# Optimization experiments

Hardware: AMD Instinct MI355X
Metric: run time of the kernel (lower is better)

The kernel has to match this reference:

```python
import jax, jax.numpy as jnp
import numpy as np

EPS_LN = 1e-5

def _ln(x, g, b):
    m = x.mean(-1, keepdims=True)
    v = jnp.var(x, axis=-1, keepdims=True)
    return (x - m) * jax.lax.rsqrt(v + EPS_LN) * g + b


def _forward(x, edge_attr, lin0_w, lin0_b, enn_w1, enn_b1, enn_g1, enn_b1n,
             enn_w2, enn_b2, enn_g2, enn_b2n, conv_bias,
             gru_w_ih, gru_w_hh, gru_b_ih, gru_b_hh,
             lstm_w_ih, lstm_w_hh, lstm_b_ih, lstm_b_hh,
             lin1_w, lin1_b, lin1_g, lin1_bn, lin2_w, lin2_b,
             edge_index, target_index, target_class):
    N = x.shape[0]
    D = lin0_w.shape[0]
    src, dst = edge_index[0], edge_index[1]

    out = jax.nn.relu(x @ lin0_w.T + lin0_b)            # [N, D]
    h = out                                             # GRU hidden state

    # edge NN -> per-edge weight matrix [E, D, D] (edge_attr constant across iters)
    e1 = jax.nn.relu(_ln(edge_attr @ enn_w1.T + enn_b1, enn_g1, enn_b1n))
    ew = _ln(e1 @ enn_w2.T + enn_b2, enn_g2, enn_b2n).reshape(-1, D, D)

    counts = jnp.clip(jax.ops.segment_sum(jnp.ones_like(dst, jnp.float32), dst, num_segments=N), 1.0)[:, None]

    for _ in range(3):
        msg = jnp.einsum('ed,edo->eo', out[src], ew)     # per-edge matmul
        agg = jax.ops.segment_sum(msg, dst, num_segments=N) / counts  # scatter-mean
        m = jax.nn.relu(agg + conv_bias)
        # GRU cell (seq len 1)
        gx = m @ gru_w_ih.T + gru_b_ih
        gh = h @ gru_w_hh.T + gru_b_hh
        xr, xz, xn = jnp.split(gx, 3, axis=-1)
        hr, hz, hn = jnp.split(gh, 3, axis=-1)
        r = jax.nn.sigmoid(xr + hr)
        z = jax.nn.sigmoid(xz + hz)
        n = jnp.tanh(xn + r * hn)
        h = (1.0 - z) * n + z * h
        out = h

    # Set2Set with batch_index = arange(N) (each node is its own set), 3 steps
    idx = jnp.arange(N)
    hl = jnp.zeros((N, D), x.dtype)
    cl = jnp.zeros((N, D), x.dtype)
    q_star = jnp.zeros((N, 2 * D), x.dtype)
    for _ in range(3):
        g = q_star @ lstm_w_ih.T + lstm_b_ih + hl @ lstm_w_hh.T + lstm_b_hh
        gi, gf, gg, go = jnp.split(g, 4, axis=-1)
        cl = jax.nn.sigmoid(gf) * cl + jax.nn.sigmoid(gi) * jnp.tanh(gg)
        hl = jax.nn.sigmoid(go) * jnp.tanh(cl)
        q = hl
        e = (out * q[idx]).sum(-1, keepdims=True)
        emax = jax.ops.segment_max(e, idx, num_segments=N)
        a = jnp.exp(e - emax[idx])
        a = a / (jax.ops.segment_sum(a, idx, num_segments=N)[idx] + 1e-16)
        r_pool = jax.ops.segment_sum(a * out, idx, num_segments=N)
        q_star = jnp.concatenate([q, r_pool], axis=-1)

    a0, a1 = target_index[0], target_index[1]
    cat = jnp.concatenate([out[a0], out[a1], q_star[a0], q_star[a1]], axis=-1)  # [P, 6D]
    p = jax.nn.relu(_ln(cat @ lin1_w.T + lin1_b, lin1_g, lin1_bn))
    p = p @ lin2_w.T + lin2_b                           # [P, 8]
    return jnp.take_along_axis(p, target_class[:, None], axis=1)[:, 0]


def setup_inputs() -> dict:
    N, E, P, F, D = 10000, 20000, 15000, 16, 64
    ks = iter(jax.random.split(jax.random.key(0), 40))
    def nrm(shape, s=0.1):
        return jax.random.normal(next(ks), shape, jnp.float32) * s
    return {
        'x': jax.random.normal(next(ks), (N, F), jnp.float32),
        'edge_attr': jax.random.normal(next(ks), (E, 4), jnp.float32),
        'lin0_w': nrm((D, F)), 'lin0_b': jnp.zeros((D,), jnp.float32),
        'enn_w1': nrm((128, 4)), 'enn_b1': jnp.zeros((128,), jnp.float32),
        'enn_g1': jnp.ones((128,), jnp.float32), 'enn_b1n': jnp.zeros((128,), jnp.float32),
        'enn_w2': nrm((D * D, 128), 0.05), 'enn_b2': jnp.zeros((D * D,), jnp.float32),
        'enn_g2': jnp.ones((D * D,), jnp.float32), 'enn_b2n': jnp.zeros((D * D,), jnp.float32),
        'conv_bias': jnp.zeros((D,), jnp.float32),
        'gru_w_ih': nrm((3 * D, D)), 'gru_w_hh': nrm((3 * D, D)),
        'gru_b_ih': jnp.zeros((3 * D,), jnp.float32), 'gru_b_hh': jnp.zeros((3 * D,), jnp.float32),
        'lstm_w_ih': nrm((4 * D, 2 * D)), 'lstm_w_hh': nrm((4 * D, D)),
        'lstm_b_ih': jnp.zeros((4 * D,), jnp.float32), 'lstm_b_hh': jnp.zeros((4 * D,), jnp.float32),
        'lin1_w': nrm((D, 6 * D)), 'lin1_b': jnp.zeros((D,), jnp.float32),
        'lin1_g': jnp.ones((D,), jnp.float32), 'lin1_bn': jnp.zeros((D,), jnp.float32),
        'lin2_w': nrm((8, D)), 'lin2_b': jnp.zeros((8,), jnp.float32),
        'edge_index': jax.random.randint(next(ks), (2, E), 0, N),
        'target_index': jax.random.randint(next(ks), (2, P), 0, N),
        'target_class': jax.random.randint(next(ks), (P,), 0, 8),
    }


def reference(x, edge_attr, lin0_w, lin0_b, enn_w1, enn_b1, enn_g1, enn_b1n,
              enn_w2, enn_b2, enn_g2, enn_b2n, conv_bias,
              gru_w_ih, gru_w_hh, gru_b_ih, gru_b_hh,
              lstm_w_ih, lstm_w_hh, lstm_b_ih, lstm_b_hh,
              lin1_w, lin1_b, lin1_g, lin1_bn, lin2_w, lin2_b,
              edge_index, target_index, target_class):
    return _forward(x, edge_attr, lin0_w, lin0_b, enn_w1, enn_b1, enn_g1, enn_b1n,
                    enn_w2, enn_b2, enn_g2, enn_b2n, conv_bias,
                    gru_w_ih, gru_w_hh, gru_b_ih, gru_b_hh,
                    lstm_w_ih, lstm_w_hh, lstm_b_ih, lstm_b_hh,
                    lin1_w, lin1_b, lin1_g, lin1_bn, lin2_w, lin2_b,
                    edge_index, target_index, target_class)
```

## Files before the change

kernel.cpp:

```cpp
#include <hip/hip_runtime.h>
#include <hip/hip_bf16.h>

#define EPS_LN 1e-5f

typedef __attribute__((ext_vector_type(8))) short bf16x8;
typedef __attribute__((ext_vector_type(4))) float f32x4;

__device__ __forceinline__ float dot4(float4 a, float4 b) {
    return a.x * b.x + a.y * b.y + a.z * b.z + a.w * b.w;
}
__device__ __forceinline__ float sigmoidf_(float x) { return 1.0f / (1.0f + expf(-x)); }

__device__ __forceinline__ float bfu2f(unsigned short u) {
    unsigned v = ((unsigned)u) << 16;
    float f;
    __builtin_memcpy(&f, &v, 4);
    return f;
}
__device__ __forceinline__ unsigned short f2bfu(float f) {
    __hip_bfloat16 h = __float2bfloat16(f);
    unsigned short u;
    __builtin_memcpy(&u, &h, 2);
    return u;
}
__device__ __forceinline__ unsigned pack2bf(float a, float b) {
    return (unsigned)f2bfu(a) | ((unsigned)f2bfu(b) << 16);
}

__global__ void init_kernel(const float* __restrict__ x, const float* __restrict__ w,
                            const float* __restrict__ b, float* __restrict__ h,
                            const int* __restrict__ ei, float* __restrict__ counts,
                            int N, int E) {
    int id = blockIdx.x * blockDim.x + threadIdx.x;
    if (id < N * 64) {
        int n = id >> 6, o = id & 63;
        const float* xr = x + n * 16;
        const float* wr = w + o * 16;
        float acc = b[o];
#pragma unroll
        for (int k = 0; k < 16; k++) acc += xr[k] * wr[k];
        h[id] = fmaxf(acc, 0.0f);
    }
    if (id < E) atomicAdd(&counts[ei[E + id]], 1.0f);
}

__global__ __launch_bounds__(128) void edge_nn1_kernel(
    const float* __restrict__ ea, const float* __restrict__ w1, const float* __restrict__ b1,
    const float* __restrict__ g1, const float* __restrict__ b1n,
    unsigned short* __restrict__ e1h, unsigned short* __restrict__ e1l, int E) {
    int e = blockIdx.x, j = threadIdx.x;
    float a0 = ea[e * 4 + 0], a1 = ea[e * 4 + 1], a2 = ea[e * 4 + 2], a3 = ea[e * 4 + 3];
    const float* wr = w1 + j * 4;
    float z = b1[j] + a0 * wr[0] + a1 * wr[1] + a2 * wr[2] + a3 * wr[3];
    float s = z, s2 = z * z;
#pragma unroll
    for (int m = 32; m >= 1; m >>= 1) { s += __shfl_xor(s, m); s2 += __shfl_xor(s2, m); }
    __shared__ float ls[2], ls2[2];
    int wv = j >> 6;
    if ((j & 63) == 0) { ls[wv] = s; ls2[wv] = s2; }
    __syncthreads();
    float S = ls[0] + ls[1], S2 = ls2[0] + ls2[1];
    float mu = S * (1.0f / 128.0f);
    float var = fmaxf(S2 * (1.0f / 128.0f) - mu * mu, 0.0f);
    float inv = rsqrtf(var + EPS_LN);
    float v = fmaxf((z - mu) * inv * g1[j] + b1n[j], 0.0f);
    unsigned short hi = f2bfu(v);
    unsigned short lo = f2bfu(v - bfu2f(hi));
    e1h[e * 128 + j] = hi;
    e1l[e * 128 + j] = lo;
}

__global__ __launch_bounds__(128) void mpart_kernel(const float* __restrict__ w2,
                                                    const float* __restrict__ b2,
                                                    const float* __restrict__ g2,
                                                    unsigned short* __restrict__ w2g,
                                                    float* __restrict__ b2g,
                                                    float* __restrict__ pMT, float* __restrict__ pv,
                                                    float* __restrict__ pcw, float* __restrict__ psb,
                                                    float* __restrict__ pc) {
    __shared__ float wL[16][128];
    __shared__ float b2L[16];
    int t = threadIdx.x, b = blockIdx.x;
#pragma unroll
    for (int i = 0; i < 16; i++) {
        int idx = t + i * 128;
        wL[idx >> 7][idx & 127] = w2[(size_t)(b * 16 + (idx >> 7)) * 128 + (idx & 127)];
    }
    if (t < 16) b2L[t] = b2[b * 16 + t];
    __syncthreads();
#pragma unroll
    for (int o = 0; o < 16; o++) {
        int row = b * 16 + o;
        w2g[(size_t)row * 128 + t] = f2bfu(wL[o][t] * g2[row]);
    }
    if (t < 16) b2g[b * 16 + t] = b2L[t] * g2[b * 16 + t];
    int j = t;
    float wj[16];
#pragma unroll
    for (int o = 0; o < 16; o++) wj[o] = wL[o][j];
    float pvj = 0.f, pcwj = 0.f;
#pragma unroll
    for (int o = 0; o < 16; o++) { pvj += wj[o] * b2L[o]; pcwj += wj[o]; }
    for (int i4 = 0; i4 < 32; i4++) {
        float4 a = {0.f, 0.f, 0.f, 0.f};
#pragma unroll
        for (int o = 0; o < 16; o++) {
            float4 w4 = *(const float4*)&wL[o][i4 * 4];
            a.x += wj[o] * w4.x; a.y += wj[o] * w4.y;
            a.z += wj[o] * w4.z; a.w += wj[o] * w4.w;
        }
        *(float4*)&pMT[((size_t)b * 128 + j) * 128 + i4 * 4] = a;
    }
    pv[b * 128 + j] = pvj;
    pcw[b * 128 + j] = pcwj;
    if (t == 0) {
        float sb = 0.f, cc = 0.f;
#pragma unroll
        for (int o = 0; o < 16; o++) { sb += b2L[o]; cc += b2L[o] * b2L[o]; }
        psb[b] = sb;
        pc[b] = cc;
    }
}

__global__ __launch_bounds__(256) void mreduce_kernel(const float* __restrict__ pMT,
                                                      const float* __restrict__ pv,
                                                      const float* __restrict__ pcw,
                                                      const float* __restrict__ psb,
                                                      const float* __restrict__ pc,
                                                      unsigned short* __restrict__ mb,
                                                      float* __restrict__ varr,
                                                      float* __restrict__ cw,
                                                      float* __restrict__ sbc) {
    int fid = blockIdx.x * 256 + threadIdx.x;
    float s = 0.f;
    int j = fid >> 7, i = fid & 127;
    for (int b = 0; b < 256; b++) s += pMT[((size_t)b * 128 + j) * 128 + i];
    mb[fid] = f2bfu(s);
    if (fid < 128) {
        float sv = 0.f, sc = 0.f;
        for (int b = 0; b < 256; b++) { sv += pv[b * 128 + fid]; sc += pcw[b * 128 + fid]; }
        varr[fid] = sv;
        cw[fid] = sc;
    }
    if (fid == 0) {
        float sb = 0.f, cc = 0.f;
        for (int b = 0; b < 256; b++) { sb += psb[b]; cc += pc[b]; }
        sbc[0] = sb;
        sbc[1] = cc;
    }
}

__global__ __launch_bounds__(256) void stats_kernel(
    const unsigned short* __restrict__ e1h, const unsigned short* __restrict__ e1l,
    const unsigned short* __restrict__ mb, const float* __restrict__ cw,
    const float* __restrict__ varr, const float* __restrict__ sbc,
    float* __restrict__ stats, int E) {
    __shared__ __align__(16) unsigned char smem[65536];
    const int t = threadIdx.x;
    const int eb = blockIdx.x * 64;
#pragma unroll
    for (int r = 0; r < 4; r++) {
        int idx = t + r * 256;
        int row = idx >> 4, kseg = idx & 15;
        int er = eb + row;
        if (er >= E) er = E - 1;
        uint4 vh = *(const uint4*)&e1h[(size_t)er * 128 + kseg * 8];
        uint4 vl = *(const uint4*)&e1l[(size_t)er * 128 + kseg * 8];
        int off = row * 256 + ((kseg * 16) ^ ((row & 7) << 4));
        *(uint4*)(smem + off) = vh;
        *(uint4*)(smem + 16384 + off) = vl;
    }
#pragma unroll
    for (int r = 0; r < 8; r++) {
        int idx = t + r * 256;
        int row = idx >> 4, kseg = idx & 15;
        uint4 v = *(const uint4*)&mb[(size_t)row * 128 + kseg * 8];
        *(uint4*)(smem + 32768 + row * 256 + ((kseg * 16) ^ ((row & 7) << 4))) = v;
    }
    __syncthreads();
    const int w = t >> 6, lane = t & 63;
    const int wrow = w * 16;
    const int r16 = lane & 15, kg = lane >> 4;
    f32x4 tacc[8];
#pragma unroll
    for (int nj = 0; nj < 8; nj++) tacc[nj] = (f32x4){0.f, 0.f, 0.f, 0.f};
#pragma unroll
    for (int ks = 0; ks < 4; ks++) {
        int arow = wrow + r16;
        int koff = ks * 64 + kg * 16;
        bf16x8 ah = *(const bf16x8*)(smem + arow * 256 + (koff ^ ((arow & 7) << 4)));
        bf16x8 al = *(const bf16x8*)(smem + 16384 + arow * 256 + (koff ^ ((arow & 7) << 4)));
#pragma unroll
        for (int nj = 0; nj < 8; nj++) {
            int brow = nj * 16 + r16;
            bf16x8 bf = *(const bf16x8*)(smem + 32768 + brow * 256 + (koff ^ ((brow & 7) << 4)));
            tacc[nj] = __builtin_amdgcn_mfma_f32_16x16x32_bf16(ah, bf, tacc[nj], 0, 0, 0);
            tacc[nj] = __builtin_amdgcn_mfma_f32_16x16x32_bf16(al, bf, tacc[nj], 0, 0, 0);
        }
    }
    __syncthreads();
#pragma unroll
    for (int nj = 0; nj < 8; nj++)
#pragma unroll
        for (int r = 0; r < 4; r++) {
            int row = wrow + kg * 4 + r, col = nj * 16 + r16;
            *(float*)(smem + 32768 + row * 512 + col * 4) = tacc[nj][r];
        }
    __syncthreads();
    int el = t >> 2, q = t & 3;
    float s2p = 0.f, sp = 0.f, svp = 0.f;
    for (int kk = 0; kk < 32; kk++) {
        int k = q * 32 + kk;
        int boff = el * 256 + ((2 * k) ^ ((el & 7) << 4));
        float e1v = bfu2f(*(const unsigned short*)(smem + boff)) +
                    bfu2f(*(const unsigned short*)(smem + 16384 + boff));
        float tv = *(const float*)(smem + 32768 + el * 512 + k * 4);
        s2p += tv * e1v;
        sp += e1v * cw[k];
        svp += e1v * varr[k];
    }
    s2p += __shfl_xor(s2p, 1); s2p += __shfl_xor(s2p, 2);
    sp += __shfl_xor(sp, 1);   sp += __shfl_xor(sp, 2);
    svp += __shfl_xor(svp, 1); svp += __shfl_xor(svp, 2);
    if (q == 0) {
        int e = eb + el;
        if (e < E) {
            float S = sp + sbc[0];
            float S2 = s2p + 2.f * svp + sbc[1];
            float mu = S * (1.0f / 4096.0f);
            float var = fmaxf(S2 * (1.0f / 4096.0f) - mu * mu, 0.0f);
            float inv = rsqrtf(var + EPS_LN);
            stats[e * 2 + 0] = inv;
            stats[e * 2 + 1] = mu * inv;
        }
    }
}

__global__ __launch_bounds__(256) void zgemm_final(
    const unsigned short* __restrict__ e1h,
    const unsigned short* __restrict__ w2g, const float* __restrict__ b2g,
    const float* __restrict__ g2, const float* __restrict__ b2n,
    const float* __restrict__ stats, unsigned short* __restrict__ zT, int E) {
    __shared__ __align__(16) unsigned char smem[49152];
    __shared__ float cBg[128], cGg[128], cBn[128];
    __shared__ float sInv[64], sMiv[64];
    const int t = threadIdx.x;
    const int eb = blockIdx.y * 64;
    const int cb = blockIdx.x * 128;
    const int o0 = blockIdx.x * 2;
#pragma unroll
    for (int r = 0; r < 4; r++) {
        int idx = t + r * 256;
        int row = idx >> 4, kseg = idx & 15;
        int er = eb + row;
        if (er >= E) er = E - 1;
        uint4 vh = *(const uint4*)&e1h[(size_t)er * 128 + kseg * 8];
        *(uint4*)(smem + row * 256 + ((kseg * 16) ^ ((row & 7) << 4))) = vh;
    }
#pragma unroll
    for (int r = 0; r < 8; r++) {
        int idx = t + r * 256;
        int j = idx >> 4, kseg = idx & 15;
        int srcrow = ((j & 63) << 6) + o0 + (j >> 6);
        uint4 v = *(const uint4*)&w2g[(size_t)srcrow * 128 + kseg * 8];
        *(uint4*)(smem + 16384 + j * 256 + ((kseg * 16) ^ ((j & 7) << 4))) = v;
    }
    if (t < 128) {
        int sj = ((t & 63) << 6) + o0 + (t >> 6);
        cBg[t] = b2g[sj];
        cGg[t] = g2[sj];
        cBn[t] = b2n[sj];
    } else if (t < 192) {
        int tt = t - 128;
        int eg = eb + tt;
        if (eg >= E) eg = E - 1;
        sInv[tt] = stats[eg * 2 + 0];
        sMiv[tt] = stats[eg * 2 + 1];
    }
    __syncthreads();
    const int w = t >> 6, lane = t & 63;
    const int wrow = (w >> 1) * 32, wcol = (w & 1) * 64;
    const int r16 = lane & 15, kg = lane >> 4;

    f32x4 acc[2][4];
#pragma unroll
    for (int mi = 0; mi < 2; mi++)
#pragma unroll
        for (int nj = 0; nj < 4; nj++) acc[mi][nj] = (f32x4){0.f, 0.f, 0.f, 0.f};
#pragma unroll
    for (int ks = 0; ks < 4; ks++) {
        int koff = ks * 64 + kg * 16;
        bf16x8 af[2];
#pragma unroll
        for (int mi = 0; mi < 2; mi++) {
            int row = wrow + mi * 16 + r16;
            af[mi] = *(const bf16x8*)(smem + row * 256 + (koff ^ ((row & 7) << 4)));
        }
        bf16x8 bf[4];
#pragma unroll
        for (int nj = 0; nj < 4; nj++) {
            int row = wcol + nj * 16 + r16;
            bf[nj] = *(const bf16x8*)(smem + 16384 + row * 256 + (koff ^ ((row & 7) << 4)));
        }
#pragma unroll
        for (int mi = 0; mi < 2; mi++)
#pragma unroll
            for (int nj = 0; nj < 4; nj++)
                acc[mi][nj] = __builtin_amdgcn_mfma_f32_16x16x32_bf16(
                    bf[nj], af[mi], acc[mi][nj], 0, 0, 0);
    }
#pragma unroll
    for (int mi = 0; mi < 2; mi++) {
        int e_local = wrow + mi * 16 + r16;
        int e = eb + e_local;
        float inv = sInv[e_local], miv = sMiv[e_local];
        bool ok = (e < E);
#pragma unroll
        for (int nj = 0; nj < 4; nj++) {
            int j0 = wcol + nj * 16 + kg * 4;
            float4 bg4 = *(const float4*)&cBg[j0];
            float4 gg4 = *(const float4*)&cGg[j0];
            float4 bn4 = *(const float4*)&cBn[j0];
            ushort4 sv;
            sv.x = f2bfu(inv * (acc[mi][nj][0] + bg4.x) - miv * gg4.x + bn4.x);
            sv.y = f2bfu(inv * (acc[mi][nj][1] + bg4.y) - miv * gg4.y + bn4.y);
            sv.z = f2bfu(inv * (acc[mi][nj][2] + bg4.z) - miv * gg4.z + bn4.z);
            sv.w = f2bfu(inv * (acc[mi][nj][3] + bg4.w) - miv * gg4.w + bn4.w);
            if (ok) *(ushort4*)&zT[(size_t)e * 4096 + cb + j0] = sv;
        }
    }
}

__global__ __launch_bounds__(256) void msg_kernel(const unsigned short* __restrict__ zT,
                                                  const float* __restrict__ h,
                                                  const int* __restrict__ ei,
                                                  float* __restrict__ agg, int E) {
    int t = threadIdx.x;
    int w = t >> 6, lane = t & 63;
    int e = blockIdx.x * 4 + w;
    __shared__ float hL[4][64];
    __shared__ float oL[4][64];
    int src = ei[e];
    int dstn = ei[E + e];
    hL[w][lane] = h[(size_t)src * 64 + lane];
    __syncthreads();
    const uint4* zp = (const uint4*)(zT + (size_t)e * 4096);
    const int d0 = (lane & 7) * 8;
    const float* hp = &hL[w][d0];
    float h0 = hp[0], h1v = hp[1], h2 = hp[2], h3 = hp[3];
    float h4 = hp[4], h5 = hp[5], h6 = hp[6], h7 = hp[7];
    float accq[8];
#pragma unroll
    for (int q = 0; q < 8; q++) {
        uint4 v = zp[q * 64 + lane];
        float a;
        a  = __uint_as_float(v.x << 16) * h0 + __uint_as_float(v.x & 0xffff0000u) * h1v;
        a += __uint_as_float(v.y << 16) * h2 + __uint_as_float(v.y & 0xffff0000u) * h3;
        a += __uint_as_float(v.z << 16) * h4 + __uint_as_float(v.z & 0xffff0000u) * h5;
        a += __uint_as_float(v.w << 16) * h6 + __uint_as_float(v.w & 0xffff0000u) * h7;
        accq[q] = a;
    }
#pragma unroll
    for (int q = 0; q < 8; q++) {
        accq[q] += __shfl_xor(accq[q], 1);
        accq[q] += __shfl_xor(accq[q], 2);
        accq[q] += __shfl_xor(accq[q], 4);
    }
    if ((lane & 7) == 0) {
#pragma unroll
        for (int q = 0; q < 8; q++) oL[w][q * 8 + (lane >> 3)] = accq[q];
    }
    __syncthreads();
    atomicAdd(&agg[(size_t)dstn * 64 + lane], oL[w][lane]);
}

__global__ __launch_bounds__(192) void gru_kernel(
    const float* __restrict__ agg, const float* __restrict__ counts, const float* __restrict__ cbias,
    const float* __restrict__ wih, const float* __restrict__ whh,
    const float* __restrict__ bih, const float* __restrict__ bhh, float* __restrict__ h, int N) {
    int t = threadIdx.x;
    int nb = blockIdx.x * 8;
    __shared__ __align__(16) float mL[8][64], hL[8][64], gxL[8][192], ghL[8][192];
    for (int idx = t; idx < 512; idx += 192) {
        int n = idx >> 6, k = idx & 63;
        int node = nb + n;
        float cnt = fmaxf(counts[node], 1.0f);
        mL[n][k] = fmaxf(agg[node * 64 + k] / cnt + cbias[k], 0.0f);
        hL[n][k] = h[node * 64 + k];
    }
    __syncthreads();
    {
        int j = t;
        float ax[8], ah[8];
#pragma unroll
        for (int n = 0; n < 8; n++) { ax[n] = 0.f; ah[n] = 0.f; }
        const float4* wi = (const float4*)(wih + j * 64);
        const float4* wh = (const float4*)(whh + j * 64);
#pragma unroll 4
        for (int k4 = 0; k4 < 16; k4++) {
            float4 wiv = wi[k4], whv = wh[k4];
#pragma unroll
            for (int n = 0; n < 8; n++) {
                ax[n] += dot4(wiv, *(const float4*)&mL[n][k4 * 4]);
                ah[n] += dot4(whv, *(const float4*)&hL[n][k4 * 4]);
            }
        }
        float bi = bih[j], bh = bhh[j];
#pragma unroll
        for (int n = 0; n < 8; n++) { gxL[n][j] = ax[n] + bi; ghL[n][j] = ah[n] + bh; }
    }
    __syncthreads();
    for (int idx = t; idx < 512; idx += 192) {
        int n = idx >> 6, k = idx & 63;
        int node = nb + n;
        float r = sigmoidf_(gxL[n][k] + ghL[n][k]);
        float zz = sigmoidf_(gxL[n][64 + k] + ghL[n][64 + k]);
        float nn = tanhf(gxL[n][128 + k] + r * ghL[n][128 + k]);
        h[node * 64 + k] = (1.0f - zz) * nn + zz * hL[n][k];
    }
}

__global__ __launch_bounds__(256) void coutprep_kernel(
    const float* __restrict__ h, const float* __restrict__ wih, const float* __restrict__ whh,
    const float* __restrict__ bih, const float* __restrict__ bhh,
    float* __restrict__ cout, float* __restrict__ wc,
    float* __restrict__ hl, float* __restrict__ cl, int N) {
    int t = threadIdx.x, nb = blockIdx.x * 8;
    __shared__ __align__(16) float oL[8][64];
    for (int idx = t; idx < 512; idx += 256) {
        int n = idx >> 6, k = idx & 63;
        oL[n][k] = h[(nb + n) * 64 + k];
    }
    __syncthreads();
    {
        float acc[8];
#pragma unroll
        for (int n = 0; n < 8; n++) acc[n] = 0.f;
        const float* wr = wih + t * 128 + 64;
#pragma unroll 4
        for (int k4 = 0; k4 < 16; k4++) {
            float4 w4 = *(const float4*)&wr[k4 * 4];
#pragma unroll
            for (int n = 0; n < 8; n++) acc[n] += dot4(w4, *(const float4*)&oL[n][k4 * 4]);
        }
#pragma unroll
        for (int n = 0; n < 8; n++) cout[(size_t)(nb + n) * 256 + t] = acc[n];
    }
    if (blockIdx.x < 64) {
        int id = blockIdx.x * 256 + t;
        int j = id >> 6, k = id & 63;
        wc[id] = wih[j * 128 + k] + whh[id];
    }
    if (t < 64) {
        float gi = bih[t] + bhh[t];
        float gg = bih[128 + t] + bhh[128 + t];
        float go = bih[192 + t] + bhh[192 + t];
        float c0 = sigmoidf_(gi) * tanhf(gg);
        float h0 = sigmoidf_(go) * tanhf(c0);
#pragma unroll
        for (int n = 0; n < 8; n++) {
            cl[(nb + n) * 64 + t] = c0;
            hl[(nb + n) * 64 + t] = h0;
        }
    }
}

__global__ __launch_bounds__(256) void lstm_step_kernel(const float* __restrict__ wc,
                                                        const float* __restrict__ bih,
                                                        const float* __restrict__ bhh,
                                                        const float* __restrict__ cout,
                                                        float* __restrict__ hl,
                                                        float* __restrict__ cl, int N) {
    int t = threadIdx.x, nb = blockIdx.x * 8;
    __shared__ __align__(16) float hlL[8][64];
    __shared__ float gL[8][256];
    for (int idx = t; idx < 512; idx += 256) {
        int n = idx >> 6, k = idx & 63;
        hlL[n][k] = hl[(nb + n) * 64 + k];
    }
    __syncthreads();
    {
        float acc[8];
#pragma unroll
        for (int n = 0; n < 8; n++) acc[n] = 0.f;
        const float4* w4p = (const float4*)(wc + t * 64);
#pragma unroll 4
        for (int k4 = 0; k4 < 16; k4++) {
            float4 w4 = w4p[k4];
#pragma unroll
            for (int n = 0; n < 8; n++) acc[n] += dot4(w4, *(const float4*)&hlL[n][k4 * 4]);
        }
        float bs = bih[t] + bhh[t];
#pragma unroll
        for (int n = 0; n < 8; n++) gL[n][t] = acc[n] + cout[(size_t)(nb + n) * 256 + t] + bs;
    }
    __syncthreads();
    for (int idx = t; idx < 512; idx += 256) {
        int n = idx >> 6, k = idx & 63;
        int node = nb + n;
        float gi = gL[n][k], gf = gL[n][64 + k], gg = gL[n][128 + k], go = gL[n][192 + k];
        float c = sigmoidf_(gf) * cl[node * 64 + k] + sigmoidf_(gi) * tanhf(gg);
        cl[node * 64 + k] = c;
        hl[node * 64 + k] = sigmoidf_(go) * tanhf(c);
    }
}

__global__ __launch_bounds__(256) void head_kernel(
    const float* __restrict__ h, const float* __restrict__ hl, const int* __restrict__ ti,
    const int* __restrict__ tc, const float* __restrict__ w1, const float* __restrict__ b1,
    const float* __restrict__ g1, const float* __restrict__ bn1, const float* __restrict__ w2,
    const float* __restrict__ b2, float* __restrict__ out, int P) {
    __shared__ uint2 w1q[6144];
    __shared__ float catL[4][384];
    int t = threadIdx.x;
    const float4* w1f4 = (const float4*)w1;
#pragma unroll
    for (int i = 0; i < 24; i++) {
        int f = t + i * 256;
        float4 v = w1f4[f];
        int j = f / 96, k4 = f - j * 96;
        w1q[k4 * 64 + j] = make_uint2(pack2bf(v.x, v.y), pack2bf(v.z, v.w));
    }
    int j = t & 63, pl = t >> 6;
    float b1j = b1[j], g1j = g1[j], bnj = bn1[j];
    __syncthreads();

    for (int pb = blockIdx.x * 4; pb < P; pb += gridDim.x * 4) {
#pragma unroll
        for (int i = 0; i < 6; i++) {
            int idx = t + i * 256;
            int p = idx / 384, kk = idx - p * 384;
            int pair = pb + p;
            if (pair >= P) pair = P - 1;
            int a0 = ti[pair], a1 = ti[P + pair];
            int s = kk >> 6, k = kk & 63;
            float v;
            if (s == 0 || s == 3) v = h[a0 * 64 + k];
            else if (s == 1 || s == 5) v = h[a1 * 64 + k];
            else if (s == 2) v = hl[a0 * 64 + k];
            else v = hl[a1 * 64 + k];
            catL[p][kk] = v;
        }
        __syncthreads();
        int pair = pb + pl;
        float acc = b1j;
#pragma unroll 8
        for (int k4 = 0; k4 < 96; k4++) {
            uint2 wv = w1q[k4 * 64 + j];
            float4 c = *(const float4*)&catL[pl][k4 * 4];
            acc += __uint_as_float(wv.x << 16) * c.x + __uint_as_float(wv.x & 0xffff0000u) * c.y;
            acc += __uint_as_float(wv.y << 16) * c.z + __uint_as_float(wv.y & 0xffff0000u) * c.w;
        }
        float s1 = acc, s2v = acc * acc;
#pragma unroll
        for (int m = 32; m >= 1; m >>= 1) { s1 += __shfl_xor(s1, m); s2v += __shfl_xor(s2v, m); }
        float mu = s1 * (1.0f / 64.0f);
        float var = fmaxf(s2v * (1.0f / 64.0f) - mu * mu, 0.0f);
        float p1 = fmaxf((acc - mu) * rsqrtf(var + EPS_LN) * g1j + bnj, 0.0f);
        int cls = tc[pair < P ? pair : P - 1];
        float part = p1 * w2[cls * 64 + j];
#pragma unroll
        for (int m = 32; m >= 1; m >>= 1) part += __shfl_xor(part, m);
        if (j == 0 && pair < P) out[pair] = part + b2[cls];
        __syncthreads();
    }
}

extern "C" void kernel_launch(void* const* d_in, const int* in_sizes, int n_in,
                              void* d_out, int out_size, void* d_ws, size_t ws_size,
                              hipStream_t stream) {
    const float* x = (const float*)d_in[0];
    const float* edge_attr = (const float*)d_in[1];
    const float* lin0_w = (const float*)d_in[2];
    const float* lin0_b = (const float*)d_in[3];
    const float* enn_w1 = (const float*)d_in[4];
    const float* enn_b1 = (const float*)d_in[5];
    const float* enn_g1 = (const float*)d_in[6];
    const float* enn_b1n = (const float*)d_in[7];
    const float* enn_w2 = (const float*)d_in[8];
    const float* enn_b2 = (const float*)d_in[9];
    const float* enn_g2 = (const float*)d_in[10];
    const float* enn_b2n = (const float*)d_in[11];
    const float* conv_bias = (const float*)d_in[12];
    const float* gru_w_ih = (const float*)d_in[13];
    const float* gru_w_hh = (const float*)d_in[14];
    const float* gru_b_ih = (const float*)d_in[15];
    const float* gru_b_hh = (const float*)d_in[16];
    const float* lstm_w_ih = (const float*)d_in[17];
    const float* lstm_w_hh = (const float*)d_in[18];
    const float* lstm_b_ih = (const float*)d_in[19];
    const float* lstm_b_hh = (const float*)d_in[20];
    const float* lin1_w = (const float*)d_in[21];
    const float* lin1_b = (const float*)d_in[22];
    const float* lin1_g = (const float*)d_in[23];
    const float* lin1_bn = (const float*)d_in[24];
    const float* lin2_w = (const float*)d_in[25];
    const float* lin2_b = (const float*)d_in[26];
    const int* edge_index = (const int*)d_in[27];
    const int* target_index = (const int*)d_in[28];
    const int* target_class = (const int*)d_in[29];

    const int N = in_sizes[0] / 16;
    const int E = in_sizes[27] / 2;
    const int P = in_sizes[29];

    size_t off = 0;
    auto carve = [&](size_t bytes) {
        void* p = (char*)d_ws + off;
        off += (bytes + 255) & ~(size_t)255;
        return p;
    };
    unsigned short* zbuf = (unsigned short*)carve((size_t)E * 4096 * 2);
    unsigned short* e1h = (unsigned short*)carve((size_t)E * 128 * 2);
    unsigned short* e1l = (unsigned short*)carve((size_t)E * 128 * 2);
    unsigned short* w2g = (unsigned short*)carve((size_t)4096 * 128 * 2);
    float* b2g = (float*)carve((size_t)4096 * 4);
    float* hbuf = (float*)carve((size_t)N * 64 * 4);
    float* counts = (float*)carve((size_t)N * 4 + (size_t)3 * N * 64 * 4);
    float* agg0 = counts + N;
    float* agg1 = agg0 + (size_t)N * 64;
    float* agg2 = agg1 + (size_t)N * 64;
    float* hl = (float*)carve((size_t)N * 64 * 4);
    float* cl = (float*)carve((size_t)N * 64 * 4);
    float* cout_b = (float*)carve((size_t)N * 256 * 4);
    float* wc = (float*)carve((size_t)256 * 64 * 4);
    float* stats = (float*)carve((size_t)E * 2 * 4);
    unsigned short* mb = (unsigned short*)carve((size_t)128 * 128 * 2);
    float* varr = (float*)carve((size_t)128 * 4);
    float* cw = (float*)carve((size_t)128 * 4);
    float* sbc = (float*)carve((size_t)2 * 4);
    float* pv = (float*)carve((size_t)256 * 128 * 4);
    float* pcw = (float*)carve((size_t)256 * 128 * 4);
    float* psb = (float*)carve((size_t)256 * 4);
    float* pc = (float*)carve((size_t)256 * 4);
    float* pMT = (float*)carve((size_t)256 * 128 * 128 * 4);
    (void)ws_size;

    hipMemsetAsync(counts, 0, (size_t)N * 4 + (size_t)3 * N * 64 * 4, stream);
    init_kernel<<<(N * 64 + 255) / 256, 256, 0, stream>>>(x, lin0_w, lin0_b, hbuf, edge_index,
                                                          counts, N, E);
    edge_nn1_kernel<<<E, 128, 0, stream>>>(edge_attr, enn_w1, enn_b1, enn_g1, enn_b1n, e1h, e1l, E);
    mpart_kernel<<<256, 128, 0, stream>>>(enn_w2, enn_b2, enn_g2, w2g, b2g, pMT, pv, pcw, psb, pc);
    mreduce_kernel<<<64, 256, 0, stream>>>(pMT, pv, pcw, psb, pc, mb, varr, cw, sbc);
    stats_kernel<<<(E + 63) / 64, 256, 0, stream>>>(e1h, e1l, mb, cw, varr, sbc, stats, E);
    {
        dim3 g(32, (E + 63) / 64);
        zgemm_final<<<g, 256, 0, stream>>>(e1h, w2g, b2g, enn_g2, enn_b2n, stats, zbuf, E);
    }

    float* aggs[3] = {agg0, agg1, agg2};
    for (int it = 0; it < 3; it++) {
        msg_kernel<<<E / 4, 256, 0, stream>>>(zbuf, hbuf, edge_index, aggs[it], E);
        gru_kernel<<<N / 8, 192, 0, stream>>>(aggs[it], counts, conv_bias, gru_w_ih, gru_w_hh,
                                              gru_b_ih, gru_b_hh, hbuf, N);
    }

    coutprep_kernel<<<N / 8, 256, 0, stream>>>(hbuf, lstm_w_ih, lstm_w_hh, lstm_b_ih, lstm_b_hh,
                                               cout_b, wc, hl, cl, N);
    lstm_step_kernel<<<N / 8, 256, 0, stream>>>(wc, lstm_b_ih, lstm_b_hh, cout_b, hl, cl, N);
    lstm_step_kernel<<<N / 8, 256, 0, stream>>>(wc, lstm_b_ih, lstm_b_hh, cout_b, hl, cl, N);

    head_kernel<<<512, 256, 0, stream>>>(hbuf, hl, target_index, target_class, lin1_w, lin1_b,
                                         lin1_g, lin1_bn, lin2_w, lin2_b, (float*)d_out, P);
}
```

Before: 385.5 us.

## Pre-swizzle e1h and w2g in global memory and load zgemm tiles via global_load_lds

```diff
diff --git a/kernel.cpp b/kernel.cpp
--- a/kernel.cpp
+++ b/kernel.cpp
@@ -25,6 +25,10 @@
 }
 __device__ __forceinline__ unsigned pack2bf(float a, float b) {
     return (unsigned)f2bfu(a) | ((unsigned)f2bfu(b) << 16);
+}
+__device__ __forceinline__ void async_cp16(void* lds, const void* g) {
+    __builtin_amdgcn_global_load_lds((const __attribute__((address_space(1))) void*)g,
+                                     (__attribute__((address_space(3))) void*)lds, 16, 0, 0);
 }
 
 __global__ void init_kernel(const float* __restrict__ x, const float* __restrict__ w,
@@ -66,14 +70,15 @@
     float v = fmaxf((z - mu) * inv * g1[j] + b1n[j], 0.0f);
     unsigned short hi = f2bfu(v);
     unsigned short lo = f2bfu(v - bfu2f(hi));
-    e1h[e * 128 + j] = hi;
-    e1l[e * 128 + j] = lo;
+    int jp = j ^ ((e & 7) << 3);
+    e1h[e * 128 + jp] = hi;
+    e1l[e * 128 + jp] = lo;
 }
 
 __global__ __launch_bounds__(128) void mpart_kernel(const float* __restrict__ w2,
                                                     const float* __restrict__ b2,
                                                     const float* __restrict__ g2,
-                                                    unsigned short* __restrict__ w2g,
+                                                    unsigned short* __restrict__ w2gp,
                                                     float* __restrict__ b2g,
                                                     float* __restrict__ pMT, float* __restrict__ pv,
                                                     float* __restrict__ pcw, float* __restrict__ psb,
@@ -90,8 +95,10 @@
     __syncthreads();
 #pragma unroll
     for (int o = 0; o < 16; o++) {
-        int row = b * 16 + o;
-        w2g[(size_t)row * 128 + t] = f2bfu(wL[o][t] * g2[row]);
+        int r = b * 16 + o;
+        int x = (r & 63) >> 1;
+        int jj = (r >> 6) + ((r & 1) << 6);
+        w2gp[(size_t)x * 16384 + jj * 128 + (t ^ ((jj & 7) << 3))] = f2bfu(wL[o][t] * g2[r]);
     }
     if (t < 16) b2g[b * 16 + t] = b2L[t] * g2[b * 16 + t];
     int j = t;
@@ -166,7 +173,7 @@
         if (er >= E) er = E - 1;
         uint4 vh = *(const uint4*)&e1h[(size_t)er * 128 + kseg * 8];
         uint4 vl = *(const uint4*)&e1l[(size_t)er * 128 + kseg * 8];
-        int off = row * 256 + ((kseg * 16) ^ ((row & 7) << 4));
+        int off = row * 256 + kseg * 16;
         *(uint4*)(smem + off) = vh;
         *(uint4*)(smem + 16384 + off) = vl;
     }
@@ -238,32 +245,26 @@
 
 __global__ __launch_bounds__(256) void zgemm_final(
     const unsigned short* __restrict__ e1h,
-    const unsigned short* __restrict__ w2g, const float* __restrict__ b2g,
+    const unsigned short* __restrict__ w2gp, const float* __restrict__ b2g,
     const float* __restrict__ g2, const float* __restrict__ b2n,
     const float* __restrict__ stats, unsigned short* __restrict__ zT, int E) {
     __shared__ __align__(16) unsigned char smem[49152];
     __shared__ float cBg[128], cGg[128], cBn[128];
     __shared__ float sInv[64], sMiv[64];
     const int t = threadIdx.x;
+    const int w = t >> 6, lane = t & 63;
     const int eb = blockIdx.y * 64;
     const int cb = blockIdx.x * 128;
     const int o0 = blockIdx.x * 2;
-#pragma unroll
-    for (int r = 0; r < 4; r++) {
-        int idx = t + r * 256;
-        int row = idx >> 4, kseg = idx & 15;
-        int er = eb + row;
-        if (er >= E) er = E - 1;
-        uint4 vh = *(const uint4*)&e1h[(size_t)er * 128 + kseg * 8];
-        *(uint4*)(smem + row * 256 + ((kseg * 16) ^ ((row & 7) << 4))) = vh;
-    }
-#pragma unroll
-    for (int r = 0; r < 8; r++) {
-        int idx = t + r * 256;
-        int j = idx >> 4, kseg = idx & 15;
-        int srcrow = ((j & 63) << 6) + o0 + (j >> 6);
-        uint4 v = *(const uint4*)&w2g[(size_t)srcrow * 128 + kseg * 8];
-        *(uint4*)(smem + 16384 + j * 256 + ((kseg * 16) ^ ((j & 7) << 4))) = v;
+    {
+        const char* srcA = (const char*)e1h + (size_t)eb * 256 + w * 1024 + lane * 16;
+        char* dstA = (char*)smem + w * 1024 + lane * 16;
+#pragma unroll
+        for (int i = 0; i < 4; i++) async_cp16(dstA + i * 4096, srcA + i * 4096);
+        const char* srcB = (const char*)w2gp + (size_t)blockIdx.x * 32768 + w * 1024 + lane * 16;
+        char* dstB = (char*)smem + 16384 + w * 1024 + lane * 16;
+#pragma unroll
+        for (int i = 0; i < 8; i++) async_cp16(dstB + i * 4096, srcB + i * 4096);
     }
     if (t < 128) {
         int sj = ((t & 63) << 6) + o0 + (t >> 6);
@@ -278,7 +279,6 @@
         sMiv[tt] = stats[eg * 2 + 1];
     }
     __syncthreads();
-    const int w = t >> 6, lane = t & 63;
     const int wrow = (w >> 1) * 32, wcol = (w & 1) * 64;
     const int r16 = lane & 15, kg = lane >> 4;
 
@@ -613,7 +613,7 @@
     unsigned short* zbuf = (unsigned short*)carve((size_t)E * 4096 * 2);
     unsigned short* e1h = (unsigned short*)carve((size_t)E * 128 * 2);
     unsigned short* e1l = (unsigned short*)carve((size_t)E * 128 * 2);
-    unsigned short* w2g = (unsigned short*)carve((size_t)4096 * 128 * 2);
+    unsigned short* w2gp = (unsigned short*)carve((size_t)4096 * 128 * 2);
     float* b2g = (float*)carve((size_t)4096 * 4);
     float* hbuf = (float*)carve((size_t)N * 64 * 4);
     float* counts = (float*)carve((size_t)N * 4 + (size_t)3 * N * 64 * 4);
@@ -640,12 +640,12 @@
     init_kernel<<<(N * 64 + 255) / 256, 256, 0, stream>>>(x, lin0_w, lin0_b, hbuf, edge_index,
                                                           counts, N, E);
     edge_nn1_kernel<<<E, 128, 0, stream>>>(edge_attr, enn_w1, enn_b1, enn_g1, enn_b1n, e1h, e1l, E);
-    mpart_kernel<<<256, 128, 0, stream>>>(enn_w2, enn_b2, enn_g2, w2g, b2g, pMT, pv, pcw, psb, pc);
+    mpart_kernel<<<256, 128, 0, stream>>>(enn_w2, enn_b2, enn_g2, w2gp, b2g, pMT, pv, pcw, psb, pc);
     mreduce_kernel<<<64, 256, 0, stream>>>(pMT, pv, pcw, psb, pc, mb, varr, cw, sbc);
     stats_kernel<<<(E + 63) / 64, 256, 0, stream>>>(e1h, e1l, mb, cw, varr, sbc, stats, E);
     {
         dim3 g(32, (E + 63) / 64);
-        zgemm_final<<<g, 256, 0, stream>>>(e1h, w2g, b2g, enn_g2, enn_b2n, stats, zbuf, E);
+        zgemm_final<<<g, 256, 0, stream>>>(e1h, w2gp, b2g, enn_g2, enn_b2n, stats, zbuf, E);
     }
 
     float* aggs[3] = {agg0, agg1, agg2};
```

Result: no change. 380.7 us (-1.3%).
